# Kernel optimization log

Measured on AMD Instinct MI355X. Metric: run time of the kernel, lower is better.

Reference implementation:

```python
import jax, jax.numpy as jnp
import numpy as np

# DynamicMaskHead config (CondLaneHead defaults, head_layers=3, channels=64)
N, INS_PER_IMG, C, H, W = 4, 8, 64, 160, 256
CIN = C + 2  # coords concatenated
L1, L2, L3 = (C + 2) * C, C * C, C * 1  # weight_nums = [4224, 4096, 64]
B1, B2, B3 = C, C, 1                     # bias_nums   = [64, 64, 1]
NUM_PARAMS = L1 + L2 + L3 + B1 + B2 + B3  # 8513
MASK_BIAS_SHIFT = 2.19  # subtracted from last bias when is_mask=True


def setup_inputs() -> dict:
    key = jax.random.key(0)
    k1, k2 = jax.random.split(key)
    x = jax.random.normal(k1, (N, C, H, W), dtype=jnp.float32)
    mask_head_params = jax.random.normal(k2, (N * INS_PER_IMG, NUM_PARAMS), dtype=jnp.float32) * 0.05
    num_ins = np.full((N,), INS_PER_IMG, dtype=np.int32)  # static per-image instance counts
    return {"x": x, "mask_head_params": mask_head_params, "num_ins": num_ins}


def _locations(h, w, dtype):
    # compute_locations with stride=1: +stride//2 == +0; original normalization
    # (locations[:0], locations[:1]) is a no-op slice, so coords stay unnormalized.
    loc_x = jnp.broadcast_to(jnp.arange(w, dtype=dtype)[None, :], (h, w))
    loc_y = jnp.broadcast_to(jnp.arange(h, dtype=dtype)[:, None], (h, w))
    return jnp.stack([loc_x, loc_y], axis=0)  # [2, H, W]


def reference(x, mask_head_params, num_ins):
    n, _, h, w = x.shape
    loc = _locations(h, w, x.dtype)
    xa = jnp.concatenate([jnp.broadcast_to(loc[None], (n, 2, h, w)), x], axis=1)  # [N, 66, H, W]

    # replicate each image's features per instance (grouped-conv input)
    img_idx = np.repeat(np.arange(n), np.asarray(num_ins))  # static
    num_insts = img_idx.shape[0]
    feats = xa[img_idx].reshape(num_insts, CIN, h * w)  # [I, 66, L]

    # parse_dynamic_params: split flat params into per-instance 1x1 conv weights/biases
    splits = jnp.split(mask_head_params, np.cumsum([L1, L2, L3, B1, B2]), axis=1)
    w0 = splits[0].reshape(num_insts, C, CIN)
    w1 = splits[1].reshape(num_insts, C, C)
    w2 = splits[2].reshape(num_insts, 1, C)
    b0 = splits[3]
    b1 = splits[4]
    b2 = splits[5] - MASK_BIAS_SHIFT  # is_mask=True

    # grouped 1x1 convs == per-instance small matmuls (batched GEMM)
    hdn = jax.nn.relu(jnp.einsum('ioc,icl->iol', w0, feats) + b0[:, :, None])
    hdn = jax.nn.relu(jnp.einsum('ioc,icl->iol', w1, hdn) + b1[:, :, None])
    out = jnp.einsum('ioc,icl->iol', w2, hdn) + b2[:, :, None]  # [I, 1, L]
    return out.reshape(1, num_insts, h, w)
```

## Files before the change

kernel.cpp:

```cpp
#include <hip/hip_runtime.h>
#include <hip/hip_bf16.h>


#define NP 8513
#define HW 40960
#define ISTRIDE 18432
#define OFF_W1 8192
#define OFF_VEC 16384

typedef __attribute__((ext_vector_type(8))) short bf16x8;
typedef __attribute__((ext_vector_type(4))) float f32x4;

__device__ inline unsigned short f2bf(float f) {
  union { float f; unsigned u; } v; v.f = f;
  unsigned r = v.u + 0x7fffu + ((v.u >> 16) & 1u);
  return (unsigned short)(r >> 16);
}
__device__ inline unsigned pk2(float a, float b) {
  __hip_bfloat162 h = __float22bfloat162_rn(float2{a, b});
  union { __hip_bfloat162 h; unsigned u; } v; v.h = h;
  return v.u;
}
__device__ inline void gld16(const void* g, void* l) {
  __builtin_amdgcn_global_load_lds(
      (const __attribute__((address_space(1))) unsigned*)g,
      (__attribute__((address_space(3))) unsigned*)l, 16, 0, 0);
}

__global__ void condlane_prep(const float* __restrict__ params,
                              char* __restrict__ ws) {
  const int inst = blockIdx.x >> 1, part = blockIdx.x & 1;
  const float* __restrict__ p = params + inst * NP;
  char* base = ws + inst * ISTRIDE;
  const int t = threadIdx.x;
  if (part == 0) {
    unsigned short* dst = (unsigned short*)base;
#pragma unroll
    for (int it = 0; it < 16; it++) {
      const int e = it * 256 + t;
      const int frag = e >> 9, lane = (e >> 3) & 63, j = e & 7;
      const int m = (frag >> 1) * 16 + (lane & 15);
      const int k = (frag & 1) * 32 + ((lane >> 4) << 3) + j;
      dst[e] = f2bf(p[m * 66 + 2 + k]);
    }
  } else {
    unsigned short* dst = (unsigned short*)(base + OFF_W1);
#pragma unroll
    for (int it = 0; it < 16; it++) {
      const int e = it * 256 + t;
      const int frag = e >> 9, lane = (e >> 3) & 63, j = e & 7;
      const int m = (frag >> 1) * 16 + (lane & 15);
      const int k = (frag & 1) * 32 + ((lane >> 4) << 3) + j;
      dst[e] = f2bf(p[4224 + m * 64 + k]);
    }
    float* vec = (float*)(base + OFF_VEC);
    if (t < 64) {
      vec[t]       = p[8384 + t];
      vec[64 + t]  = p[t * 66];
      vec[128 + t] = p[t * 66 + 1];
      vec[192 + t] = p[8448 + t];
      vec[256 + t] = p[8320 + t];
    } else if (t == 64) vec[320] = p[8512] - 2.19f;
  }
}

__global__ __launch_bounds__(256, 3) void condlane_main(
    const float* __restrict__ x, const char* __restrict__ ws,
    float* __restrict__ out) {
  __shared__ __align__(16) char smem[53248];
  const int img = blockIdx.y, bx = blockIdx.x;
  const int tid = threadIdx.x, lane = tid & 63, wave = tid >> 6;
  const int col = lane & 15, q = lane >> 4, sw = col & 7;
  const char* const wsb = ws + img * 8 * ISTRIDE;

  auto dma = [&](int i, char* buf) {
    const char* src = wsb + i * ISTRIDE;
#pragma unroll
    for (int u = 0; u < 4; u++) {
      const int off = (wave * 4 + u) * 1024;
      gld16(src + off + lane * 16, buf + off);
    }
    if (wave < 2) {
      const int off = OFF_VEC + wave * 1024;
      gld16(src + off + lane * 16, buf + off);
    }
  };
  dma(0, smem);

  bf16x8 bfr[2][2];
  {
    const float* gx = x + img * 64 * HW + bx * 128 + wave * 32;
#pragma unroll
    for (int nt = 0; nt < 2; nt++)
#pragma unroll
      for (int ks = 0; ks < 2; ks++) {
        float f[8];
#pragma unroll
        for (int j = 0; j < 8; j++)
          f[j] = gx[(ks * 32 + q * 8 + j) * HW + nt * 16 + col];
        union { bf16x8 v; unsigned d[4]; } u;
#pragma unroll
        for (int jj = 0; jj < 4; jj++) u.d[jj] = pk2(f[2 * jj], f[2 * jj + 1]);
        bfr[nt][ks] = u.v;
      }
  }
  __syncthreads();

  const float fyv = (float)(bx >> 1);
  const float fx0 = (float)((bx & 1) * 128 + wave * 32 + col);
  unsigned short* const hwv = (unsigned short*)(smem + 36864) + wave * 2048;
  float* const outb = out + img * 8 * HW + bx * 128 + wave * 32;

  for (int i = 0; i < 8; i++) {
    char* const wb = smem + (i & 1) * ISTRIDE;
    if (i < 7) dma(i + 1, smem + ((i + 1) & 1) * ISTRIDE);
    const float* const vec = (const float*)(wb + OFF_VEC);

    f32x4 acc[4][2];
#pragma unroll
    for (int mt = 0; mt < 4; mt++) {
      const int ro = mt * 16 + q * 4;
      const f32x4 b0v = *(const f32x4*)(vec + ro);
      const f32x4 wxv = *(const f32x4*)(vec + 64 + ro);
      const f32x4 wyv = *(const f32x4*)(vec + 128 + ro);
      const f32x4 byv = b0v + wyv * fyv;
      acc[mt][0] = byv + wxv * fx0;
      acc[mt][1] = byv + wxv * (fx0 + 16.0f);
    }
#pragma unroll
    for (int mt = 0; mt < 4; mt++) {
      const bf16x8 a0 = *(const bf16x8*)(wb + (mt * 2 + 0) * 1024 + lane * 16);
      const bf16x8 a1 = *(const bf16x8*)(wb + (mt * 2 + 1) * 1024 + lane * 16);
#pragma unroll
      for (int nt = 0; nt < 2; nt++) {
        f32x4 c = __builtin_amdgcn_mfma_f32_16x16x32_bf16(a0, bfr[nt][0],
                                                          acc[mt][nt], 0, 0, 0);
        acc[mt][nt] = __builtin_amdgcn_mfma_f32_16x16x32_bf16(a1, bfr[nt][1],
                                                              c, 0, 0, 0);
      }
    }
#pragma unroll
    for (int nt = 0; nt < 2; nt++)
#pragma unroll
      for (int mt = 0; mt < 4; mt++) {
        const f32x4 v = acc[mt][nt];
        uint2 dd;
        dd.x = pk2(fmaxf(v.x, 0.f), fmaxf(v.y, 0.f));
        dd.y = pk2(fmaxf(v.z, 0.f), fmaxf(v.w, 0.f));
        const int kb = (mt * 2 + (q >> 1)) ^ sw;
        *(uint2*)(hwv + nt * 1024 + col * 64 + (kb << 3) + ((q & 1) << 2)) = dd;
      }
    bf16x8 hbf[2][2];
#pragma unroll
    for (int nt = 0; nt < 2; nt++)
#pragma unroll
      for (int ks = 0; ks < 2; ks++)
        hbf[nt][ks] = *(const bf16x8*)(hwv + nt * 1024 + col * 64 +
                                       (((ks * 4 + q) ^ sw) << 3));

    float s0 = 0.f, s1 = 0.f;
#pragma unroll
    for (int mt = 0; mt < 4; mt++) {
      const bf16x8 a0 = *(const bf16x8*)(wb + OFF_W1 + (mt * 2 + 0) * 1024 + lane * 16);
      const bf16x8 a1 = *(const bf16x8*)(wb + OFF_W1 + (mt * 2 + 1) * 1024 + lane * 16);
      const int ro = mt * 16 + q * 4;
      const f32x4 cb  = *(const f32x4*)(vec + 192 + ro);
      const f32x4 w2v = *(const f32x4*)(vec + 256 + ro);
      f32x4 c0 = __builtin_amdgcn_mfma_f32_16x16x32_bf16(a0, hbf[0][0], cb, 0, 0, 0);
      const f32x4 v0 = __builtin_amdgcn_mfma_f32_16x16x32_bf16(a1, hbf[0][1], c0, 0, 0, 0);
      f32x4 c1 = __builtin_amdgcn_mfma_f32_16x16x32_bf16(a0, hbf[1][0], cb, 0, 0, 0);
      const f32x4 v1 = __builtin_amdgcn_mfma_f32_16x16x32_bf16(a1, hbf[1][1], c1, 0, 0, 0);
      s0 += w2v.x * fmaxf(v0.x, 0.f) + w2v.y * fmaxf(v0.y, 0.f) +
            w2v.z * fmaxf(v0.z, 0.f) + w2v.w * fmaxf(v0.w, 0.f);
      s1 += w2v.x * fmaxf(v1.x, 0.f) + w2v.y * fmaxf(v1.y, 0.f) +
            w2v.z * fmaxf(v1.z, 0.f) + w2v.w * fmaxf(v1.w, 0.f);
    }
    const float b2i = vec[320];
    s0 += __shfl_xor(s0, 16, 64); s0 += __shfl_xor(s0, 32, 64);
    s1 += __shfl_xor(s1, 16, 64); s1 += __shfl_xor(s1, 32, 64);
    if (lane < 32)
      outb[i * HW + q * 16 + col] = (q ? s1 : s0) + b2i;

    if (i < 7) __syncthreads();
  }
}

extern "C" void kernel_launch(void* const* d_in, const int* in_sizes, int n_in,
                              void* d_out, int out_size, void* d_ws, size_t ws_size,
                              hipStream_t stream) {
  const float* x      = (const float*)d_in[0];
  const float* params = (const float*)d_in[1];
  float* out = (float*)d_out;

  condlane_prep<<<64, 256, 0, stream>>>(params, (char*)d_ws);
  condlane_main<<<dim3(320, 4), 256, 0, stream>>>(x, (const char*)d_ws, out);
}
```

Measured before the change: 114.2 us.

## Replace LDS hidden-layer transpose with permlane swaps and split prep across more blocks

The layer-1 output is now moved into the B-operand layout for layer 2 with permlane32/permlane16 swap instructions instead of being written to and read back from an LDS scratch area. This removes 16 KB of shared memory per block, so occupancy can rise from 3 to 4 blocks per CU (launch bounds changed to match). The prep kernel is also split over 256 blocks instead of 64, so weight conversion runs with more parallelism. The risk is that the permlane mapping must exactly reproduce the old layout, and that the new occupancy target may tighten register limits.

```diff
diff --git a/kernel.cpp b/kernel.cpp
--- a/kernel.cpp
+++ b/kernel.cpp
@@ -10,6 +10,7 @@
 
 typedef __attribute__((ext_vector_type(8))) short bf16x8;
 typedef __attribute__((ext_vector_type(4))) float f32x4;
+typedef __attribute__((ext_vector_type(2))) unsigned uint2v;
 
 __device__ inline unsigned short f2bf(float f) {
   union { float f; unsigned u; } v; v.f = f;
@@ -29,15 +30,15 @@
 
 __global__ void condlane_prep(const float* __restrict__ params,
                               char* __restrict__ ws) {
-  const int inst = blockIdx.x >> 1, part = blockIdx.x & 1;
+  const int inst = blockIdx.x >> 3, part = blockIdx.x & 7;
   const float* __restrict__ p = params + inst * NP;
   char* base = ws + inst * ISTRIDE;
   const int t = threadIdx.x;
-  if (part == 0) {
+  if (part < 4) {
     unsigned short* dst = (unsigned short*)base;
 #pragma unroll
-    for (int it = 0; it < 16; it++) {
-      const int e = it * 256 + t;
+    for (int it = 0; it < 4; it++) {
+      const int e = (part * 4 + it) * 256 + t;
       const int frag = e >> 9, lane = (e >> 3) & 63, j = e & 7;
       const int m = (frag >> 1) * 16 + (lane & 15);
       const int k = (frag & 1) * 32 + ((lane >> 4) << 3) + j;
@@ -46,31 +47,33 @@
   } else {
     unsigned short* dst = (unsigned short*)(base + OFF_W1);
 #pragma unroll
-    for (int it = 0; it < 16; it++) {
-      const int e = it * 256 + t;
+    for (int it = 0; it < 4; it++) {
+      const int e = ((part - 4) * 4 + it) * 256 + t;
       const int frag = e >> 9, lane = (e >> 3) & 63, j = e & 7;
       const int m = (frag >> 1) * 16 + (lane & 15);
       const int k = (frag & 1) * 32 + ((lane >> 4) << 3) + j;
       dst[e] = f2bf(p[4224 + m * 64 + k]);
     }
-    float* vec = (float*)(base + OFF_VEC);
-    if (t < 64) {
-      vec[t]       = p[8384 + t];
-      vec[64 + t]  = p[t * 66];
-      vec[128 + t] = p[t * 66 + 1];
-      vec[192 + t] = p[8448 + t];
-      vec[256 + t] = p[8320 + t];
-    } else if (t == 64) vec[320] = p[8512] - 2.19f;
+    if (part == 4) {
+      float* vec = (float*)(base + OFF_VEC);
+      if (t < 64) {
+        vec[t]       = p[8384 + t];
+        vec[64 + t]  = p[t * 66];
+        vec[128 + t] = p[t * 66 + 1];
+        vec[192 + t] = p[8448 + t];
+        vec[256 + t] = p[8320 + t];
+      } else if (t == 64) vec[320] = p[8512] - 2.19f;
+    }
   }
 }
 
-__global__ __launch_bounds__(256, 3) void condlane_main(
+__global__ __launch_bounds__(256, 4) void condlane_main(
     const float* __restrict__ x, const char* __restrict__ ws,
     float* __restrict__ out) {
-  __shared__ __align__(16) char smem[53248];
+  __shared__ __align__(16) char smem[36864];
   const int img = blockIdx.y, bx = blockIdx.x;
   const int tid = threadIdx.x, lane = tid & 63, wave = tid >> 6;
-  const int col = lane & 15, q = lane >> 4, sw = col & 7;
+  const int col = lane & 15, q = lane >> 4;
   const char* const wsb = ws + img * 8 * ISTRIDE;
 
   auto dma = [&](int i, char* buf) {
@@ -108,7 +111,6 @@
 
   const float fyv = (float)(bx >> 1);
   const float fx0 = (float)((bx & 1) * 128 + wave * 32 + col);
-  unsigned short* const hwv = (unsigned short*)(smem + 36864) + wave * 2048;
   float* const outb = out + img * 8 * HW + bx * 128 + wave * 32;
 
   for (int i = 0; i < 8; i++) {
@@ -139,24 +141,35 @@
                                                               c, 0, 0, 0);
       }
     }
+
+    unsigned pd[2][4][2];
 #pragma unroll
     for (int nt = 0; nt < 2; nt++)
 #pragma unroll
       for (int mt = 0; mt < 4; mt++) {
         const f32x4 v = acc[mt][nt];
-        uint2 dd;
-        dd.x = pk2(fmaxf(v.x, 0.f), fmaxf(v.y, 0.f));
-        dd.y = pk2(fmaxf(v.z, 0.f), fmaxf(v.w, 0.f));
-        const int kb = (mt * 2 + (q >> 1)) ^ sw;
-        *(uint2*)(hwv + nt * 1024 + col * 64 + (kb << 3) + ((q & 1) << 2)) = dd;
-      }
+        pd[nt][mt][0] = pk2(fmaxf(v.x, 0.f), fmaxf(v.y, 0.f));
+        pd[nt][mt][1] = pk2(fmaxf(v.z, 0.f), fmaxf(v.w, 0.f));
+      }
+
     bf16x8 hbf[2][2];
 #pragma unroll
     for (int nt = 0; nt < 2; nt++)
 #pragma unroll
-      for (int ks = 0; ks < 2; ks++)
-        hbf[nt][ks] = *(const bf16x8*)(hwv + nt * 1024 + col * 64 +
-                                       (((ks * 4 + q) ^ sw) << 3));
+      for (int ks = 0; ks < 2; ks++) {
+        uint2v r0 = __builtin_amdgcn_permlane32_swap(
+            pd[nt][2 * ks][0], pd[nt][2 * ks + 1][0], false, false);
+        uint2v s0 = __builtin_amdgcn_permlane16_swap(r0[0], r0[1], false, false);
+        uint2v r1 = __builtin_amdgcn_permlane32_swap(
+            pd[nt][2 * ks][1], pd[nt][2 * ks + 1][1], false, false);
+        uint2v s1 = __builtin_amdgcn_permlane16_swap(r1[0], r1[1], false, false);
+        union { unsigned d[4]; bf16x8 v; } u;
+        u.d[0] = s0[0];
+        u.d[1] = s1[0];
+        u.d[2] = s0[1];
+        u.d[3] = s1[1];
+        hbf[nt][ks] = u.v;
+      }
 
     float s0 = 0.f, s1 = 0.f;
 #pragma unroll
@@ -192,6 +205,6 @@
   const float* params = (const float*)d_in[1];
   float* out = (float*)d_out;
 
-  condlane_prep<<<64, 256, 0, stream>>>(params, (char*)d_ws);
+  condlane_prep<<<256, 256, 0, stream>>>(params, (char*)d_ws);
   condlane_main<<<dim3(320, 4), 256, 0, stream>>>(x, (const char*)d_ws, out);
 }
```

After: 115.0 us. Within noise of the previous version (+0.7%).
